# Optimization experiments

Measured on AMD Instinct MI355X. Metric: run time of the kernel, lower is better.

The kernel has to match this reference:

```python
import jax, jax.numpy as jnp
import numpy as np

M0 = 0.3
R = 2
H = W = 64  # grid size from init_kwargs
N = H * W
B = 2


def _make_grid():
    # grid_by(lims=[[1,-1],[-1,1]], size=(64,64)): cartesian_prod of the two
    # linspaces, then columns swapped via index_select([1, 0]).
    a = jnp.linspace(1.0, -1.0, H)
    b = jnp.linspace(-1.0, 1.0, W)
    ga, gb = jnp.meshgrid(a, b, indexing='ij')
    cart = jnp.stack([ga, gb], axis=-1).reshape(N, 2)  # cartesian_prod order
    return cart[:, ::-1]  # swap columns -> [N, 2]


def setup_inputs() -> dict:
    key = jax.random.key(0)
    k1, k2 = jax.random.split(key)
    grid = _make_grid()
    # input points = grid + small jitter (avoids exactly-zero distances)
    inp = grid[None, :, :] + 0.05 * jax.random.normal(k1, (B, N, 2), dtype=jnp.float32)
    weight = jax.random.uniform(k2, (B, N), dtype=jnp.float32)
    return {"input": inp, "weight": weight, "grid": grid}


def reference(input, weight, grid):
    # --- brute-force KNN (r=2), k = N (full sort; equivalent to torch max_k path) ---
    # dist[b, j, i] = || grid_j - input_{b,i} ||_2   (note the .mT in torch knn)
    d2 = jnp.sum((grid[None, :, None, :] - input[:, None, :, :]) ** 2, axis=-1)  # [B,N,N]
    dist = jnp.sqrt(d2)
    order = jnp.argsort(dist, axis=-1)                       # ascending distance
    knn_dist = jnp.take_along_axis(dist, order, axis=-1)     # [B,N,N]
    knn_index = order                                        # indices into input points

    # --- weighted DTM ---
    weight_bound = M0 * jnp.sum(weight, axis=-1, keepdims=True)   # [B,1]
    wb = weight_bound[:, :, None]                                  # [B,1,1]
    # gather per-row weights of the sorted neighbors
    knn_weight = jax.vmap(lambda w, idx: w[idx])(weight, knn_index)  # [B,N,N]
    cum_knn_weight = jnp.cumsum(knn_weight, axis=-1)
    # searchsorted (left): first index where cumulative weight >= bound
    k_index = jnp.sum(cum_knn_weight < wb, axis=-1, keepdims=True)   # [B,N,1]
    k_index = jnp.minimum(k_index, N - 1)

    r_dist = knn_dist ** 2  # r == 2
    cum_dist = jnp.cumsum(r_dist * knn_weight, axis=-1)
    dtm_val = jnp.take_along_axis(
        cum_dist + r_dist * (wb - cum_knn_weight), k_index, axis=-1
    ).squeeze(-1)                                                    # [B,N]
    return jnp.sqrt(dtm_val / weight_bound)
```

## Files before the change

### kernel.cpp

```cpp
#include <hip/hip_runtime.h>
#include <math.h>

namespace {

constexpr int   kN       = 4096;
constexpr int   kThreads = 256;
constexpr int   kWPB     = kThreads / 64;
constexpr int   kEPT     = kN / 64;
constexpr int   kGroups  = kEPT / 2;
constexpr int   kIters   = 10;
constexpr float kM0      = 0.3f;
constexpr float kS       = 2048.f;
constexpr float kRootS   = 45.25483399593904f;

typedef _Float16 h2 __attribute__((ext_vector_type(2)));

__device__ __forceinline__ float waveReduceSum(float v) {
#pragma unroll
    for (int off = 32; off >= 1; off >>= 1) v += __shfl_xor(v, off);
    return v;
}

__global__ __launch_bounds__(kThreads)
void dtm_kernel(const float* __restrict__ input,
                const float* __restrict__ weight,
                const float* __restrict__ grid,
                float* __restrict__ out,
                int nq) {
    const int lane = threadIdx.x & 63;
    const int wave = threadIdx.x >> 6;
    const int q = blockIdx.x * kWPB + wave;
    if (q >= nq) return;
    const int b = q >> 12;
    const int i = q & (kN - 1);

    const float sgx = kRootS * grid[2 * i];
    const float sgy = kRootS * grid[2 * i + 1];
    const float4* inp4 = (const float4*)(input + (size_t)b * kN * 2);
    const float4* wgt4 = (const float4*)(weight + (size_t)b * kN);

    h2 d2s[kGroups], ws[kGroups];
    float wl0 = 0.f, wl1 = 0.f;
#pragma unroll
    for (int s = 0; s < kGroups / 2; ++s) {
        const int g = lane + 64 * s;
        const float4 wv = wgt4[g];
        const float4 pa = inp4[2 * g];
        const float4 pb = inp4[2 * g + 1];
        float dx, dy, d0, d1, d2_, d3;
        dx = fmaf(-kRootS, pa.x, sgx); dy = fmaf(-kRootS, pa.y, sgy); d0  = fmaf(dy, dy, dx * dx);
        dx = fmaf(-kRootS, pa.z, sgx); dy = fmaf(-kRootS, pa.w, sgy); d1  = fmaf(dy, dy, dx * dx);
        dx = fmaf(-kRootS, pb.x, sgx); dy = fmaf(-kRootS, pb.y, sgy); d2_ = fmaf(dy, dy, dx * dx);
        dx = fmaf(-kRootS, pb.z, sgx); dy = fmaf(-kRootS, pb.w, sgy); d3  = fmaf(dy, dy, dx * dx);
        d2s[2 * s]     = h2{(_Float16)d0,  (_Float16)d1};
        d2s[2 * s + 1] = h2{(_Float16)d2_, (_Float16)d3};
        ws[2 * s]      = h2{(_Float16)wv.x, (_Float16)wv.y};
        ws[2 * s + 1]  = h2{(_Float16)wv.z, (_Float16)wv.w};
        wl0 += wv.x + wv.y;
        wl1 += wv.z + wv.w;
    }
    const float wb = kM0 * waveReduceSum(wl0 + wl1);

    const h2 zero2 = h2{(_Float16)0.f, (_Float16)0.f};
    const h2 one2  = h2{(_Float16)1.f, (_Float16)1.f};

    float lo = 0.f, hi = 32768.f;
#pragma unroll
    for (int it = 0; it < kIters; ++it) {
        const float mid = 0.5f * (lo + hi);
        const _Float16 mh = (_Float16)mid;
        const h2 mid2 = h2{mh, mh};
        float a0 = 0.f, a1 = 0.f, a2 = 0.f, a3 = 0.f;
#pragma unroll
        for (int g = 0; g < kGroups; g += 4) {
            h2 t0 = mid2 - d2s[g + 0];
            h2 t1 = mid2 - d2s[g + 1];
            h2 t2 = mid2 - d2s[g + 2];
            h2 t3 = mid2 - d2s[g + 3];
            t0 = __builtin_elementwise_min(__builtin_elementwise_max(t0, zero2), one2);
            t1 = __builtin_elementwise_min(__builtin_elementwise_max(t1, zero2), one2);
            t2 = __builtin_elementwise_min(__builtin_elementwise_max(t2, zero2), one2);
            t3 = __builtin_elementwise_min(__builtin_elementwise_max(t3, zero2), one2);
            a0 = __builtin_amdgcn_fdot2(ws[g + 0], t0, a0, false);
            a1 = __builtin_amdgcn_fdot2(ws[g + 1], t1, a1, false);
            a2 = __builtin_amdgcn_fdot2(ws[g + 2], t2, a2, false);
            a3 = __builtin_amdgcn_fdot2(ws[g + 3], t3, a3, false);
        }
        const float T = waveReduceSum((a0 + a1) + (a2 + a3));
        if (T >= wb) hi = mid; else lo = mid;
    }

    {
        const _Float16 lh = (_Float16)lo;
        const h2 lo2 = h2{lh, lh};
        float W0 = 0.f, W1 = 0.f, A0 = 0.f, A1 = 0.f;
#pragma unroll
        for (int g = 0; g < kGroups; g += 2) {
            h2 t0 = lo2 - d2s[g + 0];
            h2 t1 = lo2 - d2s[g + 1];
            t0 = __builtin_elementwise_min(__builtin_elementwise_max(t0, zero2), one2);
            t1 = __builtin_elementwise_min(__builtin_elementwise_max(t1, zero2), one2);
            const h2 p0 = d2s[g + 0] * ws[g + 0];
            const h2 p1 = d2s[g + 1] * ws[g + 1];
            W0 = __builtin_amdgcn_fdot2(ws[g + 0], t0, W0, false);
            W1 = __builtin_amdgcn_fdot2(ws[g + 1], t1, W1, false);
            A0 = __builtin_amdgcn_fdot2(p0, t0, A0, false);
            A1 = __builtin_amdgcn_fdot2(p1, t1, A1, false);
        }
        const float W = waveReduceSum(W0 + W1);
        const float A = waveReduceSum(A0 + A1);
        if (lane == 0) {
            const float dtm = (A + hi * (wb - W)) * (1.f / kS);
            out[q] = sqrtf(fmaxf(dtm, 0.f) / wb);
        }
    }
}

}

extern "C" void kernel_launch(void* const* d_in, const int* in_sizes, int n_in,
                              void* d_out, int out_size, void* d_ws, size_t ws_size,
                              hipStream_t stream) {
    const float* input  = (const float*)d_in[0];
    const float* weight = (const float*)d_in[1];
    const float* grid   = (const float*)d_in[2];
    float* out = (float*)d_out;
    const int nq = out_size;
    const int blocks = (nq + kWPB - 1) / kWPB;
    dtm_kernel<<<dim3(blocks), dim3(kThreads), 0, stream>>>(input, weight, grid, out, nq);
}
```

Baseline: 81.92 us.

## Use DPP wave reductions, clamped packed subtract, fewer bisection iterations, reuse lower sum

Replaces the shuffle-based wave reductions with DPP row operations plus a readlane. Fuses the packed-f16 subtract and clamp into one v_pk_add_f16 with the clamp modifier, and converts with cvt_pkrtz. Cuts the bisection from 10 to 9 iterations and reuses the last lower-bound mass instead of recomputing W in the final pass, which removes one reduction and one dot chain. It also adds a launch-bounds occupancy hint. Fewer iterations and round-toward-zero conversion may change accuracy. Tlo stays 0 if no midpoint ever goes below the bound, which may not match the previous W.

```diff
diff --git a/kernel.cpp b/kernel.cpp
--- a/kernel.cpp
+++ b/kernel.cpp
@@ -5,23 +5,46 @@
 
 constexpr int   kN       = 4096;
 constexpr int   kThreads = 256;
-constexpr int   kWPB     = kThreads / 64;
-constexpr int   kEPT     = kN / 64;
-constexpr int   kGroups  = kEPT / 2;
-constexpr int   kIters   = 10;
+constexpr int   kGroups  = 32;
+constexpr int   kIters   = 9;
 constexpr float kM0      = 0.3f;
 constexpr float kS       = 2048.f;
 constexpr float kRootS   = 45.25483399593904f;
 
 typedef _Float16 h2 __attribute__((ext_vector_type(2)));
 
-__device__ __forceinline__ float waveReduceSum(float v) {
-#pragma unroll
-    for (int off = 32; off >= 1; off >>= 1) v += __shfl_xor(v, off);
-    return v;
+__device__ __forceinline__ h2 pkrtz(float a, float b) {
+    return __builtin_bit_cast(h2, __builtin_amdgcn_cvt_pkrtz(a, b));
 }
 
-__global__ __launch_bounds__(kThreads)
+__device__ __forceinline__ float dppAdd_(float x, int t) {
+    return x + __builtin_bit_cast(float, t);
+}
+__device__ __forceinline__ float waveSumUniform(float x) {
+    int xi;
+    xi = __builtin_amdgcn_update_dpp(0, __builtin_bit_cast(int, x), 0x111, 0xf, 0xf, true);
+    x  = dppAdd_(x, xi);
+    xi = __builtin_amdgcn_update_dpp(0, __builtin_bit_cast(int, x), 0x112, 0xf, 0xf, true);
+    x  = dppAdd_(x, xi);
+    xi = __builtin_amdgcn_update_dpp(0, __builtin_bit_cast(int, x), 0x114, 0xf, 0xf, true);
+    x  = dppAdd_(x, xi);
+    xi = __builtin_amdgcn_update_dpp(0, __builtin_bit_cast(int, x), 0x118, 0xf, 0xf, true);
+    x  = dppAdd_(x, xi);
+    xi = __builtin_amdgcn_update_dpp(0, __builtin_bit_cast(int, x), 0x142, 0xa, 0xf, true);
+    x  = dppAdd_(x, xi);
+    xi = __builtin_amdgcn_update_dpp(0, __builtin_bit_cast(int, x), 0x143, 0xc, 0xf, true);
+    x  = dppAdd_(x, xi);
+    return __builtin_bit_cast(float, __builtin_amdgcn_readlane(__builtin_bit_cast(int, x), 63));
+}
+
+__device__ __forceinline__ h2 subClamp01(h2 m, h2 d) {
+    h2 r;
+    asm("v_pk_add_f16 %0, %1, %2 neg_lo:[0,1] neg_hi:[0,1] clamp"
+        : "=v"(r) : "v"(m), "v"(d));
+    return r;
+}
+
+__global__ __launch_bounds__(kThreads, 4)
 void dtm_kernel(const float* __restrict__ input,
                 const float* __restrict__ weight,
                 const float* __restrict__ grid,
@@ -29,7 +52,7 @@
                 int nq) {
     const int lane = threadIdx.x & 63;
     const int wave = threadIdx.x >> 6;
-    const int q = blockIdx.x * kWPB + wave;
+    const int q = blockIdx.x * 4 + wave;
     if (q >= nq) return;
     const int b = q >> 12;
     const int i = q & (kN - 1);
@@ -39,78 +62,65 @@
     const float4* inp4 = (const float4*)(input + (size_t)b * kN * 2);
     const float4* wgt4 = (const float4*)(weight + (size_t)b * kN);
 
+    const h2 one2 = h2{(_Float16)1.f, (_Float16)1.f};
+
     h2 d2s[kGroups], ws[kGroups];
-    float wl0 = 0.f, wl1 = 0.f;
+    float wl = 0.f;
 #pragma unroll
     for (int s = 0; s < kGroups / 2; ++s) {
         const int g = lane + 64 * s;
         const float4 wv = wgt4[g];
         const float4 pa = inp4[2 * g];
         const float4 pb = inp4[2 * g + 1];
-        float dx, dy, d0, d1, d2_, d3;
-        dx = fmaf(-kRootS, pa.x, sgx); dy = fmaf(-kRootS, pa.y, sgy); d0  = fmaf(dy, dy, dx * dx);
-        dx = fmaf(-kRootS, pa.z, sgx); dy = fmaf(-kRootS, pa.w, sgy); d1  = fmaf(dy, dy, dx * dx);
-        dx = fmaf(-kRootS, pb.x, sgx); dy = fmaf(-kRootS, pb.y, sgy); d2_ = fmaf(dy, dy, dx * dx);
-        dx = fmaf(-kRootS, pb.z, sgx); dy = fmaf(-kRootS, pb.w, sgy); d3  = fmaf(dy, dy, dx * dx);
-        d2s[2 * s]     = h2{(_Float16)d0,  (_Float16)d1};
-        d2s[2 * s + 1] = h2{(_Float16)d2_, (_Float16)d3};
-        ws[2 * s]      = h2{(_Float16)wv.x, (_Float16)wv.y};
-        ws[2 * s + 1]  = h2{(_Float16)wv.z, (_Float16)wv.w};
-        wl0 += wv.x + wv.y;
-        wl1 += wv.z + wv.w;
+        float dx, dy, e0, e1, e2, e3;
+        dx = fmaf(-kRootS, pa.x, sgx); dy = fmaf(-kRootS, pa.y, sgy); e0 = fmaf(dy, dy, dx * dx);
+        dx = fmaf(-kRootS, pa.z, sgx); dy = fmaf(-kRootS, pa.w, sgy); e1 = fmaf(dy, dy, dx * dx);
+        dx = fmaf(-kRootS, pb.x, sgx); dy = fmaf(-kRootS, pb.y, sgy); e2 = fmaf(dy, dy, dx * dx);
+        dx = fmaf(-kRootS, pb.z, sgx); dy = fmaf(-kRootS, pb.w, sgy); e3 = fmaf(dy, dy, dx * dx);
+        d2s[2 * s]     = pkrtz(e0, e1);
+        d2s[2 * s + 1] = pkrtz(e2, e3);
+        ws[2 * s]      = pkrtz(wv.x, wv.y);
+        ws[2 * s + 1]  = pkrtz(wv.z, wv.w);
+        wl = __builtin_amdgcn_fdot2(ws[2 * s],     one2, wl, false);
+        wl = __builtin_amdgcn_fdot2(ws[2 * s + 1], one2, wl, false);
+        if ((s & 1) == 1) asm volatile("" ::: "memory");
     }
-    const float wb = kM0 * waveReduceSum(wl0 + wl1);
+    const float wb = kM0 * waveSumUniform(wl);
 
-    const h2 zero2 = h2{(_Float16)0.f, (_Float16)0.f};
-    const h2 one2  = h2{(_Float16)1.f, (_Float16)1.f};
-
-    float lo = 0.f, hi = 32768.f;
+    float lo = 0.f, hi = 32768.f, Tlo = 0.f;
 #pragma unroll
     for (int it = 0; it < kIters; ++it) {
         const float mid = 0.5f * (lo + hi);
         const _Float16 mh = (_Float16)mid;
         const h2 mid2 = h2{mh, mh};
-        float a0 = 0.f, a1 = 0.f, a2 = 0.f, a3 = 0.f;
+        float a0 = 0.f, a1 = 0.f;
 #pragma unroll
-        for (int g = 0; g < kGroups; g += 4) {
-            h2 t0 = mid2 - d2s[g + 0];
-            h2 t1 = mid2 - d2s[g + 1];
-            h2 t2 = mid2 - d2s[g + 2];
-            h2 t3 = mid2 - d2s[g + 3];
-            t0 = __builtin_elementwise_min(__builtin_elementwise_max(t0, zero2), one2);
-            t1 = __builtin_elementwise_min(__builtin_elementwise_max(t1, zero2), one2);
-            t2 = __builtin_elementwise_min(__builtin_elementwise_max(t2, zero2), one2);
-            t3 = __builtin_elementwise_min(__builtin_elementwise_max(t3, zero2), one2);
-            a0 = __builtin_amdgcn_fdot2(ws[g + 0], t0, a0, false);
+        for (int g = 0; g < kGroups; g += 2) {
+            const h2 t0 = subClamp01(mid2, d2s[g]);
+            const h2 t1 = subClamp01(mid2, d2s[g + 1]);
+            a0 = __builtin_amdgcn_fdot2(ws[g],     t0, a0, false);
             a1 = __builtin_amdgcn_fdot2(ws[g + 1], t1, a1, false);
-            a2 = __builtin_amdgcn_fdot2(ws[g + 2], t2, a2, false);
-            a3 = __builtin_amdgcn_fdot2(ws[g + 3], t3, a3, false);
         }
-        const float T = waveReduceSum((a0 + a1) + (a2 + a3));
-        if (T >= wb) hi = mid; else lo = mid;
+        const float T = waveSumUniform(a0 + a1);
+        if (T >= wb) hi = mid; else { lo = mid; Tlo = T; }
     }
 
     {
         const _Float16 lh = (_Float16)lo;
         const h2 lo2 = h2{lh, lh};
-        float W0 = 0.f, W1 = 0.f, A0 = 0.f, A1 = 0.f;
+        float A0 = 0.f, A1 = 0.f;
 #pragma unroll
         for (int g = 0; g < kGroups; g += 2) {
-            h2 t0 = lo2 - d2s[g + 0];
-            h2 t1 = lo2 - d2s[g + 1];
-            t0 = __builtin_elementwise_min(__builtin_elementwise_max(t0, zero2), one2);
-            t1 = __builtin_elementwise_min(__builtin_elementwise_max(t1, zero2), one2);
-            const h2 p0 = d2s[g + 0] * ws[g + 0];
+            const h2 t0 = subClamp01(lo2, d2s[g]);
+            const h2 t1 = subClamp01(lo2, d2s[g + 1]);
+            const h2 p0 = d2s[g] * ws[g];
             const h2 p1 = d2s[g + 1] * ws[g + 1];
-            W0 = __builtin_amdgcn_fdot2(ws[g + 0], t0, W0, false);
-            W1 = __builtin_amdgcn_fdot2(ws[g + 1], t1, W1, false);
             A0 = __builtin_amdgcn_fdot2(p0, t0, A0, false);
             A1 = __builtin_amdgcn_fdot2(p1, t1, A1, false);
         }
-        const float W = waveReduceSum(W0 + W1);
-        const float A = waveReduceSum(A0 + A1);
+        const float A = waveSumUniform(A0 + A1);
         if (lane == 0) {
-            const float dtm = (A + hi * (wb - W)) * (1.f / kS);
+            const float dtm = (A + hi * (wb - Tlo)) * (1.f / kS);
             out[q] = sqrtf(fmaxf(dtm, 0.f) / wb);
         }
     }
@@ -126,6 +136,6 @@
     const float* grid   = (const float*)d_in[2];
     float* out = (float*)d_out;
     const int nq = out_size;
-    const int blocks = (nq + kWPB - 1) / kWPB;
+    const int blocks = (nq + 3) / 4;
     dtm_kernel<<<dim3(blocks), dim3(kThreads), 0, stream>>>(input, weight, grid, out, nq);
 }
```

Result: faster. 75.73 us (-7.6%).
